# Kernel tuning notes

Hardware: AMD Instinct MI355X
Metric: run time of the kernel (lower is better)

The kernel has to match this reference:

```python
import jax, jax.numpy as jnp
import numpy as np

B, T, K, H = 4, 2048, 128, 8
MASK = True


def setup_inputs() -> dict:
    key = jax.random.key(0)
    ks = jax.random.split(key, 6)
    s = 0.02
    return {
        "x": jax.random.normal(ks[0], (B, T, K), dtype=jnp.float32),
        "Wq": jax.random.normal(ks[1], (K, H * K), dtype=jnp.float32) * s,
        "Wk": jax.random.normal(ks[2], (K, H * K), dtype=jnp.float32) * s,
        "Wv": jax.random.normal(ks[3], (K, H * K), dtype=jnp.float32) * s,
        "Wu": jax.random.normal(ks[4], (H * K, K), dtype=jnp.float32) * s,
        "bu": jnp.zeros((K,), dtype=jnp.float32),
    }


def reference(x, Wq, Wk, Wv, Wu, bu):
    b, t, k = x.shape
    h = H
    q = (x @ Wq).reshape(b, t, h, k)
    kk = (x @ Wk).reshape(b, t, h, k)
    # module pre-scales values by k**-0.25 (idiosyncratic but faithful)
    v = (x @ Wv).reshape(b, t, h, k) * (k ** -0.25)
    # scores [b, h, t, t], scaled by k**-0.5
    scores = jnp.einsum('bthd,bshd->bhts', q, kk) * (k ** -0.5)
    if MASK:
        causal = jnp.tril(jnp.ones((t, t), dtype=bool))
        scores = jnp.where(causal, scores, -jnp.inf)
    w = jax.nn.softmax(scores, axis=-1)
    out = jnp.einsum('bhts,bshd->bthd', w, v).reshape(b, t, h * k)
    return out @ Wu + bu
```

## Files before the change

kernel.cpp:

```cpp
#include <hip/hip_runtime.h>
#include <hip/hip_bf16.h>
#include <math.h>

#define B_ 4
#define T_ 2048
#define D_ 128
#define H_ 8
#define BT_ 8192
#define HD_ 1024

typedef __attribute__((ext_vector_type(8))) short bf16x8;
typedef __attribute__((ext_vector_type(4))) float f32x4;

__device__ __forceinline__ short f2bf(float f) {
  union { float f; unsigned u; } v; v.f = f;
  return (short)((v.u + 0x8000u) >> 16);
}

#if __has_builtin(__builtin_amdgcn_exp2f)
#define EXP2F(x) __builtin_amdgcn_exp2f(x)
#else
#define EXP2F(x) exp2f(x)
#endif

#define QSCALE 0.12752040242046492f
#define VSCALE 0.29730177875068026f

__device__ __forceinline__ void gld16(const short* g, short* l) {
  __builtin_amdgcn_global_load_lds(
      (const __attribute__((address_space(1))) void*)g,
      (__attribute__((address_space(3))) void*)l, 16, 0, 0);
}

__global__ __launch_bounds__(256) void prep(
    const float* __restrict__ x, const float* __restrict__ Wq,
    const float* __restrict__ Wk, const float* __restrict__ Wv,
    short* __restrict__ xbf, short* __restrict__ WT)
{
  __shared__ __align__(16) short Tt[128*128];
  const int tid = threadIdx.x;
  const int id = blockIdx.x;
  if (id < 24) {
    const int wsel = id >> 3, nt = id & 7;
    const float* W = (wsel == 0) ? Wq : (wsel == 1) ? Wk : Wv;
    #pragma unroll 4
    for (int i = tid; i < 4096; i += 256) {
      int k = i >> 5, n4 = (i & 31) << 2;
      float4 v = *(const float4*)&W[(size_t)k * HD_ + nt*128 + n4];
      float vv[4] = {v.x, v.y, v.z, v.w};
      #pragma unroll
      for (int j = 0; j < 4; j++) {
        int n = n4 + j;
        Tt[n*128 + (((k >> 3) ^ (n & 15)) << 3) + (k & 7)] = f2bf(vv[j]);
      }
    }
    __syncthreads();
    short* dst = WT + (size_t)id * 16384;
    #pragma unroll 2
    for (int i = tid; i < 2048; i += 256)
      *(bf16x8*)&dst[i*8] = *(bf16x8*)&Tt[i*8];
  } else {
    const int xb = id - 24;
    const float* xs = x + (size_t)xb * 16384;
    short* dst = xbf + (size_t)xb * 16384;
    #pragma unroll 4
    for (int i = tid; i < 4096; i += 256) {
      float4 v = ((const float4*)xs)[i];
      int row = i >> 5, c = (i & 31) >> 1, half = i & 1;
      short4 p;
      p.x = f2bf(v.x); p.y = f2bf(v.y); p.z = f2bf(v.z); p.w = f2bf(v.w);
      *(short4*)&dst[(row*16 + (c ^ (row & 15)))*8 + half*4] = p;
    }
  }
}

__global__ __launch_bounds__(256, 2) void qkv_proj(
    const short* __restrict__ xbf, const short* __restrict__ WT,
    short* __restrict__ Qw, short* __restrict__ Kw, short* __restrict__ Vw)
{
  __shared__ __align__(16) short As[16384];
  __shared__ __align__(16) short Bs[16384];
  const int tid = threadIdx.x;
  const int w = tid >> 6, lane = tid & 63, quad = lane >> 4, l16 = lane & 15;
  const int m0 = blockIdx.x * 128;

  {
    const short* asrc = xbf + (size_t)blockIdx.x * 16384;
    const short* bsrc = WT + (size_t)blockIdx.y * 16384;
    const int so = w*4096 + lane*8;
    #pragma unroll
    for (int cc = 0; cc < 8; cc++) {
      gld16(asrc + so + cc*512, &As[w*4096 + cc*512]);
      gld16(bsrc + so + cc*512, &Bs[w*4096 + cc*512]);
    }
  }
  __syncthreads();

  const int wm = (w & 1) * 64, wn = (w >> 1) * 64;
  f32x4 acc[4][4];
  #pragma unroll
  for (int a = 0; a < 4; a++)
    #pragma unroll
    for (int b = 0; b < 4; b++) acc[a][b] = (f32x4){0.f, 0.f, 0.f, 0.f};

  #pragma unroll
  for (int kk = 0; kk < 4; kk++) {
    const int swz = ((kk*4 + quad) ^ l16) << 3;
    bf16x8 af[4], bfv[4];
    #pragma unroll
    for (int mi = 0; mi < 4; mi++) af[mi]  = *(bf16x8*)&As[(wm + mi*16 + l16)*128 + swz];
    #pragma unroll
    for (int ni = 0; ni < 4; ni++) bfv[ni] = *(bf16x8*)&Bs[(wn + ni*16 + l16)*128 + swz];
    #pragma unroll
    for (int mi = 0; mi < 4; mi++)
      #pragma unroll
      for (int ni = 0; ni < 4; ni++)
        acc[mi][ni] = __builtin_amdgcn_mfma_f32_16x16x32_bf16(af[mi], bfv[ni], acc[mi][ni], 0, 0, 0);
  }

  __syncthreads();
  const int wsel = (int)blockIdx.y >> 3;
  #pragma unroll
  for (int mi = 0; mi < 4; mi++) {
    #pragma unroll
    for (int ni = 0; ni < 4; ni++) {
      const int t0l = wm + mi*16 + quad*4;
      const int d   = wn + ni*16 + l16;
      if (wsel == 0) {
        #pragma unroll
        for (int r = 0; r < 4; r++)
          As[(t0l + r)*128 + d] = f2bf(acc[mi][ni][r] * QSCALE);
      } else if (wsel == 1) {
        const int c = d >> 3;
        #pragma unroll
        for (int r = 0; r < 4; r++) {
          const int tl = (t0l + r) & 63, tile = (t0l + r) >> 6;
          As[tile*8192 + tl*128 + ((c ^ (tl & 15)) << 3) + (d & 7)] =
              f2bf(acc[mi][ni][r]);
        }
      } else {
        #pragma unroll
        for (int r = 0; r < 4; r++) {
          const int tl = (t0l + r) & 63, tile = (t0l + r) >> 6;
          As[tile*8192 + d*64 + (((tl >> 3) ^ (d & 7)) << 3) + (tl & 7)] =
              f2bf(acc[mi][ni][r] * VSCALE);
        }
      }
    }
  }
  __syncthreads();

  const int h = (int)blockIdx.y & 7;
  const int b = m0 >> 11, t0 = m0 & 2047;
  short* base = ((wsel == 0) ? Qw : (wsel == 1) ? Kw : Vw)
              + (size_t)(b*H_ + h)*262144 + (size_t)t0*128;
  #pragma unroll 2
  for (int i = tid; i < 2048; i += 256)
    *(bf16x8*)&base[i*8] = *(bf16x8*)&As[i*8];
}

__global__ __launch_bounds__(256, 2) void attn_kernel(
    const short* __restrict__ Qw, const short* __restrict__ Kw,
    const short* __restrict__ Vw, short* __restrict__ attnw)
{
  __shared__ __align__(16) short Ks[2][8192];
  __shared__ __align__(16) short Vs[2][8192];
  __shared__ __align__(16) short Ps[4096];

  const int tid = threadIdx.x;
  const int id = (int)blockIdx.x;
  const int xcd = id & 7;
  const int u   = (id >> 3) & 3;
  const int pid = id >> 5;
  const int bh = xcd | (u << 3);
  const int b = bh >> 3, h = bh & 7;
  const int w = tid >> 6, lane = tid & 63, quad = lane >> 4, l16 = lane & 15;

  const short* Qp = Qw + (size_t)bh * T_ * D_;
  const short* Kp = Kw + (size_t)bh * T_ * D_;
  const short* Vp = Vw + (size_t)bh * D_ * T_;
  short* Pw = &Ps[w*1024];
  const int so = w*2048 + lane*8;

  #pragma unroll 1
  for (int ph = 0; ph < 2; ph++) {
    const int qi = ph ? (31 - pid) : pid;
    const int rowQ = qi*64 + w*16;

    bf16x8 qa[4];
    #pragma unroll
    for (int kk = 0; kk < 4; kk++)
      qa[kk] = *(const bf16x8*)(Qp + (size_t)(rowQ + l16)*D_ + kk*32 + quad*8);

    f32x4 o[8];
    #pragma unroll
    for (int e = 0; e < 8; e++) o[e] = (f32x4){0,0,0,0};
    float l[4] = {0,0,0,0};

    __syncthreads();
    {
      const short* kt = Kp;
      const short* vt = Vp;
      #pragma unroll
      for (int cc = 0; cc < 4; cc++) {
        gld16(kt + so + cc*512, &Ks[0][w*2048 + cc*512]);
        gld16(vt + so + cc*512, &Vs[0][w*2048 + cc*512]);
      }
    }
    int buf = 0;

    for (int it = 0; it <= qi; ++it) {
      __syncthreads();
      if (it < qi) {
        const short* kt = Kp + ((size_t)(it+1) << 13);
        const short* vt = Vp + ((size_t)(it+1) << 13);
        #pragma unroll
        for (int cc = 0; cc < 4; cc++) {
          gld16(kt + so + cc*512, &Ks[buf^1][w*2048 + cc*512]);
          gld16(vt + so + cc*512, &Vs[buf^1][w*2048 + cc*512]);
        }
      }
      const short* ks = &Ks[buf][0];
      const short* vs = &Vs[buf][0];

      f32x4 s[4];
      #pragma unroll
      for (int nj = 0; nj < 4; nj++) s[nj] = (f32x4){0,0,0,0};
      #pragma unroll
      for (int kk = 0; kk < 4; kk++) {
        const int swz = ((kk*4 + quad) ^ l16) << 3;
        #pragma unroll
        for (int nj = 0; nj < 4; nj++) {
          bf16x8 kb = *(const bf16x8*)&ks[(nj*16 + l16)*128 + swz];
          s[nj] = __builtin_amdgcn_mfma_f32_16x16x32_bf16(qa[kk], kb, s[nj], 0, 0, 0);
        }
      }

      if (it < qi) {
        #pragma unroll
        for (int nj = 0; nj < 4; nj++) {
          #pragma unroll
          for (int r = 0; r < 4; r++) {
            float p = EXP2F(s[nj][r]);
            l[r] += p;
            const int row = quad*4 + r, col = nj*16 + l16;
            Pw[row*64 + (((col >> 3) ^ (row & 7)) << 3) + (col & 7)] = f2bf(p);
          }
        }
      } else {
        const int s0 = it * 64;
        #pragma unroll
        for (int nj = 0; nj < 4; nj++) {
          const int key = s0 + nj*16 + l16;
          #pragma unroll
          for (int r = 0; r < 4; r++) {
            float p = (key > rowQ + quad*4 + r) ? 0.f : EXP2F(s[nj][r]);
            l[r] += p;
            const int row = quad*4 + r, col = nj*16 + l16;
            Pw[row*64 + (((col >> 3) ^ (row & 7)) << 3) + (col & 7)] = f2bf(p);
          }
        }
      }

      #pragma unroll
      for (int kk2 = 0; kk2 < 2; kk2++) {
        const int swz = ((kk2*4 + quad) ^ (l16 & 7)) << 3;
        bf16x8 pa = *(bf16x8*)&Pw[l16*64 + swz];
        #pragma unroll
        for (int e = 0; e < 8; e++) {
          bf16x8 vb = *(const bf16x8*)&vs[(e*16 + l16)*64 + swz];
          o[e] = __builtin_amdgcn_mfma_f32_16x16x32_bf16(pa, vb, o[e], 0, 0, 0);
        }
      }
      buf ^= 1;
    }

    #pragma unroll
    for (int r = 0; r < 4; r++) {
      float t = l[r];
      t += __shfl_xor(t, 1); t += __shfl_xor(t, 2);
      t += __shfl_xor(t, 4); t += __shfl_xor(t, 8);
      l[r] = 1.0f / t;
    }
    const size_t tb = ((size_t)((b*2048 + rowQ) >> 5) * 8 + h) * 4096;
    const int row0 = rowQ & 31;
    #pragma unroll
    for (int e = 0; e < 8; e++) {
      const int c = e*2 + (l16 >> 3);
      #pragma unroll
      for (int r = 0; r < 4; r++) {
        const int row = row0 + quad*4 + r;
        attnw[tb + row*128 + ((c ^ (row & 15)) << 3) + (l16 & 7)] =
            f2bf(o[e][r] * l[r]);
      }
    }
  }
}

__global__ __launch_bounds__(256) void wu_prep(
    const float* __restrict__ Wu, short* __restrict__ WuT)
{
  __shared__ __align__(16) short Tt[128*128];
  const int tid = threadIdx.x;
  const int kc = blockIdx.x;
  #pragma unroll 4
  for (int i = tid; i < 4096; i += 256) {
    int kl = i >> 5, n4 = (i & 31) << 2;
    float4 v = *(const float4*)&Wu[(size_t)(kc*128 + kl) * D_ + n4];
    float vv[4] = {v.x, v.y, v.z, v.w};
    #pragma unroll
    for (int j = 0; j < 4; j++) {
      int n = n4 + j;
      Tt[n*128 + (((kl >> 3) ^ (n & 15)) << 3) + (kl & 7)] = f2bf(vv[j]);
    }
  }
  __syncthreads();
  short* dst = WuT + (size_t)kc * 16384;
  #pragma unroll 2
  for (int i = tid; i < 2048; i += 256)
    *(bf16x8*)&dst[i*8] = *(bf16x8*)&Tt[i*8];
}

__global__ __launch_bounds__(256, 2) void out_proj(
    const short* __restrict__ attnw, const short* __restrict__ WuT,
    const float* __restrict__ bu, float* __restrict__ out)
{
  __shared__ __align__(16) short As2[2][2048];
  __shared__ __align__(16) short Bs2[2][16384];
  const int tid = threadIdx.x;
  const int w = tid >> 6, lane = tid & 63, quad = lane >> 4, l16 = lane & 15;
  const int m0 = (int)blockIdx.x * 16;
  const int mtile32 = m0 >> 5, half = (m0 >> 4) & 1;

  f32x4 o2[2];
  o2[0] = (f32x4){0,0,0,0}; o2[1] = (f32x4){0,0,0,0};

  {
    const short* ab = attnw + (size_t)(mtile32*8 + 0)*4096 + half*2048;
    const short* bb = WuT;
    gld16(ab + w*512 + lane*8, &As2[0][w*512]);
    #pragma unroll
    for (int cc = 0; cc < 8; cc++)
      gld16(bb + w*4096 + cc*512 + lane*8, &Bs2[0][w*4096 + cc*512]);
  }
  int buf = 0;

  for (int kc = 0; kc < 8; kc++) {
    __syncthreads();
    if (kc < 7) {
      const short* ab = attnw + (size_t)(mtile32*8 + kc + 1)*4096 + half*2048;
      const short* bb = WuT + (size_t)(kc + 1)*16384;
      gld16(ab + w*512 + lane*8, &As2[buf^1][w*512]);
      #pragma unroll
      for (int cc = 0; cc < 8; cc++)
        gld16(bb + w*4096 + cc*512 + lane*8, &Bs2[buf^1][w*4096 + cc*512]);
    }
    const short* as = &As2[buf][0];
    const short* bs = &Bs2[buf][0];
    #pragma unroll
    for (int kk = 0; kk < 4; kk++) {
      const int swz = ((kk*4 + quad) ^ l16) << 3;
      bf16x8 a = *(const bf16x8*)&as[l16*128 + swz];
      #pragma unroll
      for (int e = 0; e < 2; e++) {
        bf16x8 bfr = *(const bf16x8*)&bs[((w*2 + e)*16 + l16)*128 + swz];
        o2[e] = __builtin_amdgcn_mfma_f32_16x16x32_bf16(a, bfr, o2[e], 0, 0, 0);
      }
    }
    buf ^= 1;
  }

  #pragma unroll
  for (int e = 0; e < 2; e++) {
    const int n = (w*2 + e)*16 + l16;
    const float bias = bu[n];
    #pragma unroll
    for (int r = 0; r < 4; r++) {
      const int m = m0 + quad*4 + r;
      out[(size_t)m*D_ + n] = o2[e][r] + bias;
    }
  }
}

extern "C" void kernel_launch(void* const* d_in, const int* in_sizes, int n_in,
                              void* d_out, int out_size, void* d_ws, size_t ws_size,
                              hipStream_t stream) {
  (void)in_sizes; (void)n_in; (void)out_size; (void)ws_size;
  const float* x  = (const float*)d_in[0];
  const float* Wq = (const float*)d_in[1];
  const float* Wk = (const float*)d_in[2];
  const float* Wv = (const float*)d_in[3];
  const float* Wu = (const float*)d_in[4];
  const float* bu = (const float*)d_in[5];
  float* out = (float*)d_out;

  const size_t headElems = (size_t)B_ * H_ * T_ * D_;
  short* Qw    = (short*)d_ws;
  short* Kw    = Qw + headElems;
  short* Vw    = Kw + headElems;
  short* attnw = Vw + headElems;
  short* xbf = attnw;
  short* WT  = attnw + 1048576;
  short* WuT = Kw;

  prep<<<dim3(88), 256, 0, stream>>>(x, Wq, Wk, Wv, xbf, WT);
  qkv_proj<<<dim3(64, 24), 256, 0, stream>>>(xbf, WT, Qw, Kw, Vw);
  attn_kernel<<<dim3(512), 256, 0, stream>>>(Qw, Kw, Vw, attnw);
  wu_prep<<<dim3(8), 256, 0, stream>>>(Wu, WuT);
  out_proj<<<dim3(512), 256, 0, stream>>>(attnw, WuT, bu, out);
}
```

Before: 160.3 us.

## Split attention work per query tile, single-buffer KV, split-K out projection

The Q layout from the projection now uses the same swizzled tile layout as K. The attention kernel changes from two balanced query tiles per block with double-buffered K/V to one query tile per block across twice as many blocks. It drops double buffering to cut LDS, raises the occupancy hint to 4 blocks per CU, and stages output through LDS for coalesced stores. The output projection becomes a 128-row tile GEMM split four ways over heads, writing fp32 partials that a new reduce kernel sums and adds bias to. The goals are better occupancy and fewer weight reloads, at the cost of losing load/compute overlap in attention and adding an extra pass over the partials.

```diff
diff --git a/kernel.cpp b/kernel.cpp
--- a/kernel.cpp
+++ b/kernel.cpp
@@ -126,17 +126,14 @@
     for (int ni = 0; ni < 4; ni++) {
       const int t0l = wm + mi*16 + quad*4;
       const int d   = wn + ni*16 + l16;
-      if (wsel == 0) {
-        #pragma unroll
-        for (int r = 0; r < 4; r++)
-          As[(t0l + r)*128 + d] = f2bf(acc[mi][ni][r] * QSCALE);
-      } else if (wsel == 1) {
+      if (wsel <= 1) {
+        const float sc = wsel ? 1.0f : QSCALE;
         const int c = d >> 3;
         #pragma unroll
         for (int r = 0; r < 4; r++) {
           const int tl = (t0l + r) & 63, tile = (t0l + r) >> 6;
           As[tile*8192 + tl*128 + ((c ^ (tl & 15)) << 3) + (d & 7)] =
-              f2bf(acc[mi][ni][r]);
+              f2bf(acc[mi][ni][r] * sc);
         }
       } else {
         #pragma unroll
@@ -159,141 +156,141 @@
     *(bf16x8*)&base[i*8] = *(bf16x8*)&As[i*8];
 }
 
-__global__ __launch_bounds__(256, 2) void attn_kernel(
+__global__ __launch_bounds__(256, 4) void attn_kernel(
     const short* __restrict__ Qw, const short* __restrict__ Kw,
     const short* __restrict__ Vw, short* __restrict__ attnw)
 {
-  __shared__ __align__(16) short Ks[2][8192];
-  __shared__ __align__(16) short Vs[2][8192];
+  __shared__ __align__(16) short Ks[8192];
+  __shared__ __align__(16) short Vs[8192];
   __shared__ __align__(16) short Ps[4096];
 
   const int tid = threadIdx.x;
   const int id = (int)blockIdx.x;
   const int xcd = id & 7;
-  const int u   = (id >> 3) & 3;
-  const int pid = id >> 5;
+  const int j   = id >> 3;
+  const int u   = j & 3;
+  const int q   = (j >> 2) & 7;
+  const int vv  = (j >> 5) & 3;
+  const int slot = u ^ vv;
+  const int qi = (slot == 0) ? q : (slot == 1) ? 15 - q
+               : (slot == 2) ? 16 + q : 31 - q;
   const int bh = xcd | (u << 3);
   const int b = bh >> 3, h = bh & 7;
   const int w = tid >> 6, lane = tid & 63, quad = lane >> 4, l16 = lane & 15;
-
-  const short* Qp = Qw + (size_t)bh * T_ * D_;
-  const short* Kp = Kw + (size_t)bh * T_ * D_;
-  const short* Vp = Vw + (size_t)bh * D_ * T_;
+  const int rowQ = qi*64 + w*16;
+
+  const short* Qp = Qw + (size_t)bh * 262144;
+  const short* Kp = Kw + (size_t)bh * 262144;
+  const short* Vp = Vw + (size_t)bh * 262144;
+
+  bf16x8 qa[4];
+  {
+    const int tl = (rowQ & 63) + l16;
+    const short* qp = Qp + ((size_t)(rowQ >> 6) << 13) + tl*128;
+    #pragma unroll
+    for (int kk = 0; kk < 4; kk++)
+      qa[kk] = *(const bf16x8*)(qp + (((kk*4 + quad) ^ (tl & 15)) << 3));
+  }
+
+  f32x4 o[8];
+  #pragma unroll
+  for (int e = 0; e < 8; e++) o[e] = (f32x4){0,0,0,0};
+  float l[4] = {0,0,0,0};
+
   short* Pw = &Ps[w*1024];
   const int so = w*2048 + lane*8;
-
-  #pragma unroll 1
-  for (int ph = 0; ph < 2; ph++) {
-    const int qi = ph ? (31 - pid) : pid;
-    const int rowQ = qi*64 + w*16;
-
-    bf16x8 qa[4];
-    #pragma unroll
-    for (int kk = 0; kk < 4; kk++)
-      qa[kk] = *(const bf16x8*)(Qp + (size_t)(rowQ + l16)*D_ + kk*32 + quad*8);
-
-    f32x4 o[8];
-    #pragma unroll
-    for (int e = 0; e < 8; e++) o[e] = (f32x4){0,0,0,0};
-    float l[4] = {0,0,0,0};
-
+  const int nIter = qi + 1;
+
+  for (int it = 0; it < nIter; ++it) {
+    if (it) __syncthreads();
+    {
+      const short* kt = Kp + ((size_t)it << 13);
+      const short* vt = Vp + ((size_t)it << 13);
+      #pragma unroll
+      for (int cc = 0; cc < 4; cc++) {
+        gld16(kt + so + cc*512, &Ks[w*2048 + cc*512]);
+        gld16(vt + so + cc*512, &Vs[w*2048 + cc*512]);
+      }
+    }
     __syncthreads();
-    {
-      const short* kt = Kp;
-      const short* vt = Vp;
-      #pragma unroll
-      for (int cc = 0; cc < 4; cc++) {
-        gld16(kt + so + cc*512, &Ks[0][w*2048 + cc*512]);
-        gld16(vt + so + cc*512, &Vs[0][w*2048 + cc*512]);
-      }
-    }
-    int buf = 0;
-
-    for (int it = 0; it <= qi; ++it) {
-      __syncthreads();
-      if (it < qi) {
-        const short* kt = Kp + ((size_t)(it+1) << 13);
-        const short* vt = Vp + ((size_t)(it+1) << 13);
+
+    f32x4 s[4];
+    #pragma unroll
+    for (int nj = 0; nj < 4; nj++) s[nj] = (f32x4){0,0,0,0};
+    #pragma unroll
+    for (int kk = 0; kk < 4; kk++) {
+      const int swz = ((kk*4 + quad) ^ l16) << 3;
+      #pragma unroll
+      for (int nj = 0; nj < 4; nj++) {
+        bf16x8 kb = *(const bf16x8*)&Ks[(nj*16 + l16)*128 + swz];
+        s[nj] = __builtin_amdgcn_mfma_f32_16x16x32_bf16(qa[kk], kb, s[nj], 0, 0, 0);
+      }
+    }
+
+    if (it < qi) {
+      #pragma unroll
+      for (int nj = 0; nj < 4; nj++) {
         #pragma unroll
-        for (int cc = 0; cc < 4; cc++) {
-          gld16(kt + so + cc*512, &Ks[buf^1][w*2048 + cc*512]);
-          gld16(vt + so + cc*512, &Vs[buf^1][w*2048 + cc*512]);
+        for (int r = 0; r < 4; r++) {
+          float p = EXP2F(s[nj][r]);
+          l[r] += p;
+          const int row = quad*4 + r, col = nj*16 + l16;
+          Pw[row*64 + (((col >> 3) ^ (row & 7)) << 3) + (col & 7)] = f2bf(p);
         }
       }
-      const short* ks = &Ks[buf][0];
-      const short* vs = &Vs[buf][0];
-
-      f32x4 s[4];
-      #pragma unroll
-      for (int nj = 0; nj < 4; nj++) s[nj] = (f32x4){0,0,0,0};
-      #pragma unroll
-      for (int kk = 0; kk < 4; kk++) {
-        const int swz = ((kk*4 + quad) ^ l16) << 3;
+    } else {
+      const int s0 = it * 64;
+      #pragma unroll
+      for (int nj = 0; nj < 4; nj++) {
+        const int key = s0 + nj*16 + l16;
         #pragma unroll
-        for (int nj = 0; nj < 4; nj++) {
-          bf16x8 kb = *(const bf16x8*)&ks[(nj*16 + l16)*128 + swz];
-          s[nj] = __builtin_amdgcn_mfma_f32_16x16x32_bf16(qa[kk], kb, s[nj], 0, 0, 0);
+        for (int r = 0; r < 4; r++) {
+          float p = (key > rowQ + quad*4 + r) ? 0.f : EXP2F(s[nj][r]);
+          l[r] += p;
+          const int row = quad*4 + r, col = nj*16 + l16;
+          Pw[row*64 + (((col >> 3) ^ (row & 7)) << 3) + (col & 7)] = f2bf(p);
         }
       }
-
-      if (it < qi) {
-        #pragma unroll
-        for (int nj = 0; nj < 4; nj++) {
-          #pragma unroll
-          for (int r = 0; r < 4; r++) {
-            float p = EXP2F(s[nj][r]);
-            l[r] += p;
-            const int row = quad*4 + r, col = nj*16 + l16;
-            Pw[row*64 + (((col >> 3) ^ (row & 7)) << 3) + (col & 7)] = f2bf(p);
-          }
-        }
-      } else {
-        const int s0 = it * 64;
-        #pragma unroll
-        for (int nj = 0; nj < 4; nj++) {
-          const int key = s0 + nj*16 + l16;
-          #pragma unroll
-          for (int r = 0; r < 4; r++) {
-            float p = (key > rowQ + quad*4 + r) ? 0.f : EXP2F(s[nj][r]);
-            l[r] += p;
-            const int row = quad*4 + r, col = nj*16 + l16;
-            Pw[row*64 + (((col >> 3) ^ (row & 7)) << 3) + (col & 7)] = f2bf(p);
-          }
-        }
-      }
-
-      #pragma unroll
-      for (int kk2 = 0; kk2 < 2; kk2++) {
-        const int swz = ((kk2*4 + quad) ^ (l16 & 7)) << 3;
-        bf16x8 pa = *(bf16x8*)&Pw[l16*64 + swz];
-        #pragma unroll
-        for (int e = 0; e < 8; e++) {
-          bf16x8 vb = *(const bf16x8*)&vs[(e*16 + l16)*64 + swz];
-          o[e] = __builtin_amdgcn_mfma_f32_16x16x32_bf16(pa, vb, o[e], 0, 0, 0);
-        }
-      }
-      buf ^= 1;
-    }
-
+    }
+
+    #pragma unroll
+    for (int kk2 = 0; kk2 < 2; kk2++) {
+      const int swz = ((kk2*4 + quad) ^ (l16 & 7)) << 3;
+      bf16x8 pa = *(bf16x8*)&Pw[l16*64 + swz];
+      #pragma unroll
+      for (int e = 0; e < 8; e++) {
+        bf16x8 vb = *(const bf16x8*)&Vs[(e*16 + l16)*64 + swz];
+        o[e] = __builtin_amdgcn_mfma_f32_16x16x32_bf16(pa, vb, o[e], 0, 0, 0);
+      }
+    }
+  }
+
+  #pragma unroll
+  for (int r = 0; r < 4; r++) {
+    float t = l[r];
+    t += __shfl_xor(t, 1); t += __shfl_xor(t, 2);
+    t += __shfl_xor(t, 4); t += __shfl_xor(t, 8);
+    l[r] = 1.0f / t;
+  }
+  __syncthreads();
+  #pragma unroll
+  for (int e = 0; e < 8; e++) {
+    const int c = e*2 + (l16 >> 3);
     #pragma unroll
     for (int r = 0; r < 4; r++) {
-      float t = l[r];
-      t += __shfl_xor(t, 1); t += __shfl_xor(t, 2);
-      t += __shfl_xor(t, 4); t += __shfl_xor(t, 8);
-      l[r] = 1.0f / t;
-    }
-    const size_t tb = ((size_t)((b*2048 + rowQ) >> 5) * 8 + h) * 4096;
-    const int row0 = rowQ & 31;
-    #pragma unroll
-    for (int e = 0; e < 8; e++) {
-      const int c = e*2 + (l16 >> 3);
-      #pragma unroll
-      for (int r = 0; r < 4; r++) {
-        const int row = row0 + quad*4 + r;
-        attnw[tb + row*128 + ((c ^ (row & 15)) << 3) + (l16 & 7)] =
-            f2bf(o[e][r] * l[r]);
-      }
-    }
+      const int lrow = w*16 + quad*4 + r;
+      const int sub = lrow >> 5, r32 = lrow & 31;
+      Ks[sub*4096 + r32*128 + ((c ^ (r32 & 15)) << 3) + (l16 & 7)] =
+          f2bf(o[e][r] * l[r]);
+    }
+  }
+  __syncthreads();
+  const int st0 = b*64 + qi*2;
+  #pragma unroll 2
+  for (int i = tid; i < 1024; i += 256) {
+    const int sub = i >> 9, rem = i & 511;
+    short* dst = attnw + ((size_t)(st0 + sub)*8 + h)*4096 + rem*8;
+    *(bf16x8*)dst = *(const bf16x8*)&Ks[i*8];
   }
 }
 
@@ -321,64 +318,108 @@
     *(bf16x8*)&dst[i*8] = *(bf16x8*)&Tt[i*8];
 }
 
-__global__ __launch_bounds__(256, 2) void out_proj(
+__global__ __launch_bounds__(256) void out_proj(
     const short* __restrict__ attnw, const short* __restrict__ WuT,
-    const float* __restrict__ bu, float* __restrict__ out)
-{
-  __shared__ __align__(16) short As2[2][2048];
-  __shared__ __align__(16) short Bs2[2][16384];
+    float* __restrict__ pws)
+{
+  __shared__ __align__(16) short As3[2][16384];
+  __shared__ __align__(16) short Bs3[2][16384];
   const int tid = threadIdx.x;
   const int w = tid >> 6, lane = tid & 63, quad = lane >> 4, l16 = lane & 15;
-  const int m0 = (int)blockIdx.x * 16;
-  const int mtile32 = m0 >> 5, half = (m0 >> 4) & 1;
-
-  f32x4 o2[2];
-  o2[0] = (f32x4){0,0,0,0}; o2[1] = (f32x4){0,0,0,0};
+  const int m0 = (int)blockIdx.x * 128;
+  const int kq = (int)blockIdx.y;
+  const int st0 = m0 >> 5;
+
+  f32x4 acc[2][8];
+  #pragma unroll
+  for (int mi = 0; mi < 2; mi++)
+    #pragma unroll
+    for (int ni = 0; ni < 8; ni++) acc[mi][ni] = (f32x4){0,0,0,0};
 
   {
-    const short* ab = attnw + (size_t)(mtile32*8 + 0)*4096 + half*2048;
-    const short* bb = WuT;
-    gld16(ab + w*512 + lane*8, &As2[0][w*512]);
-    #pragma unroll
-    for (int cc = 0; cc < 8; cc++)
-      gld16(bb + w*4096 + cc*512 + lane*8, &Bs2[0][w*4096 + cc*512]);
-  }
-  int buf = 0;
-
-  for (int kc = 0; kc < 8; kc++) {
+    const int hc = kq*2;
+    const short* ab = attnw + ((size_t)(st0 + w)*8 + hc)*4096;
+    const short* bb = WuT + (size_t)hc*16384 + w*4096;
+    #pragma unroll
+    for (int cc = 0; cc < 8; cc++) {
+      gld16(ab + cc*512 + lane*8, &As3[0][w*4096 + cc*512]);
+      gld16(bb + cc*512 + lane*8, &Bs3[0][w*4096 + cc*512]);
+    }
+  }
+
+  #pragma unroll
+  for (int c = 0; c < 2; c++) {
     __syncthreads();
-    if (kc < 7) {
-      const short* ab = attnw + (size_t)(mtile32*8 + kc + 1)*4096 + half*2048;
-      const short* bb = WuT + (size_t)(kc + 1)*16384;
-      gld16(ab + w*512 + lane*8, &As2[buf^1][w*512]);
-      #pragma unroll
-      for (int cc = 0; cc < 8; cc++)
-        gld16(bb + w*4096 + cc*512 + lane*8, &Bs2[buf^1][w*4096 + cc*512]);
-    }
-    const short* as = &As2[buf][0];
-    const short* bs = &Bs2[buf][0];
+    if (c == 0) {
+      const int hc = kq*2 + 1;
+      const short* ab = attnw + ((size_t)(st0 + w)*8 + hc)*4096;
+      const short* bb = WuT + (size_t)hc*16384 + w*4096;
+      #pragma unroll
+      for (int cc = 0; cc < 8; cc++) {
+        gld16(ab + cc*512 + lane*8, &As3[1][w*4096 + cc*512]);
+        gld16(bb + cc*512 + lane*8, &Bs3[1][w*4096 + cc*512]);
+      }
+    }
+    const short* as = &As3[c][0];
+    const short* bs = &Bs3[c][0];
     #pragma unroll
     for (int kk = 0; kk < 4; kk++) {
-      const int swz = ((kk*4 + quad) ^ l16) << 3;
-      bf16x8 a = *(const bf16x8*)&as[l16*128 + swz];
-      #pragma unroll
-      for (int e = 0; e < 2; e++) {
-        bf16x8 bfr = *(const bf16x8*)&bs[((w*2 + e)*16 + l16)*128 + swz];
-        o2[e] = __builtin_amdgcn_mfma_f32_16x16x32_bf16(a, bfr, o2[e], 0, 0, 0);
-      }
-    }
-    buf ^= 1;
-  }
-
-  #pragma unroll
-  for (int e = 0; e < 2; e++) {
-    const int n = (w*2 + e)*16 + l16;
-    const float bias = bu[n];
-    #pragma unroll
-    for (int r = 0; r < 4; r++) {
-      const int m = m0 + quad*4 + r;
-      out[(size_t)m*D_ + n] = o2[e][r] + bias;
-    }
+      bf16x8 a[2], bf[8];
+      #pragma unroll
+      for (int mi = 0; mi < 2; mi++) {
+        const int r32 = mi*16 + l16;
+        a[mi] = *(const bf16x8*)&as[w*4096 + r32*128 +
+                                    (((kk*4 + quad) ^ (r32 & 15)) << 3)];
+      }
+      #pragma unroll
+      for (int ni = 0; ni < 8; ni++) {
+        const int n = ni*16 + l16;
+        bf[ni] = *(const bf16x8*)&bs[n*128 + (((kk*4 + quad) ^ (n & 15)) << 3)];
+      }
+      #pragma unroll
+      for (int mi = 0; mi < 2; mi++)
+        #pragma unroll
+        for (int ni = 0; ni < 8; ni++)
+          acc[mi][ni] = __builtin_amdgcn_mfma_f32_16x16x32_bf16(a[mi], bf[ni], acc[mi][ni], 0, 0, 0);
+    }
+  }
+
+  float* dst = pws + (size_t)kq * (BT_ * D_);
+  #pragma unroll
+  for (int mi = 0; mi < 2; mi++) {
+    #pragma unroll
+    for (int ni = 0; ni < 8; ni++) {
+      const int n = ni*16 + l16;
+      #pragma unroll
+      for (int r = 0; r < 4; r++) {
+        const int m = m0 + w*32 + mi*16 + quad*4 + r;
+        dst[(size_t)m*D_ + n] = acc[mi][ni][r];
+      }
+    }
+  }
+}
+
+__global__ __launch_bounds__(256) void reduce_bias(
+    const float* __restrict__ pws, const float* __restrict__ bu,
+    float* __restrict__ out)
+{
+  const int base = ((int)blockIdx.x * 256 + (int)threadIdx.x) * 2;
+  const float4* p0 = (const float4*)pws;
+  const float4* p1 = p0 + (BT_ * D_ / 4);
+  const float4* p2 = p1 + (BT_ * D_ / 4);
+  const float4* p3 = p2 + (BT_ * D_ / 4);
+  const float4* b4 = (const float4*)bu;
+  float4* o4 = (float4*)out;
+  #pragma unroll
+  for (int j = 0; j < 2; j++) {
+    int i = base + j;
+    float4 a = p0[i], b = p1[i], c = p2[i], d = p3[i], e = b4[i & 31];
+    float4 r;
+    r.x = a.x + b.x + c.x + d.x + e.x;
+    r.y = a.y + b.y + c.y + d.y + e.y;
+    r.z = a.z + b.z + c.z + d.z + e.z;
+    r.w = a.w + b.w + c.w + d.w + e.w;
+    o4[i] = r;
   }
 }
 
@@ -402,10 +443,12 @@
   short* xbf = attnw;
   short* WT  = attnw + 1048576;
   short* WuT = Kw;
+  float* pws = (float*)Qw;
 
   prep<<<dim3(88), 256, 0, stream>>>(x, Wq, Wk, Wv, xbf, WT);
   qkv_proj<<<dim3(64, 24), 256, 0, stream>>>(xbf, WT, Qw, Kw, Vw);
-  attn_kernel<<<dim3(512), 256, 0, stream>>>(Qw, Kw, Vw, attnw);
+  attn_kernel<<<dim3(1024), 256, 0, stream>>>(Qw, Kw, Vw, attnw);
   wu_prep<<<dim3(8), 256, 0, stream>>>(Wu, WuT);
-  out_proj<<<dim3(512), 256, 0, stream>>>(attnw, WuT, bu, out);
-}
+  out_proj<<<dim3(64, 4), 256, 0, stream>>>(attnw, WuT, pws);
+  reduce_bias<<<dim3(512), 256, 0, stream>>>(pws, bu, out);
+}
```

New measurement: 166.5 us. +3.9%, slower.
